# Optimization experiments

Measured on AMD Instinct MI355X. Metric: run time of the kernel, lower is better.

The kernel has to match this reference:

```python
import jax, jax.numpy as jnp
import numpy as np

T1 = -0.075410217
T2 = 0.0
T3 = 0.062207676


def my_squash2(s_j):
    # s_j: [B, 1, C, O, 1]; piecewise-linear rescale based on sorted channel-0 magnitudes.
    B, _, C, O, _ = s_j.shape
    f = s_j[:, 0, :, 0, 0]                      # [B, C] first element of each capsule
    order = jnp.argsort(f, axis=1)
    srt = jnp.take_along_axis(f, order, axis=1)  # ascending sort per sample
    i1 = jnp.sum(srt < T1, axis=1, keepdims=True)
    i2 = jnp.sum(srt < T2, axis=1, keepdims=True)
    i3 = jnp.sum(srt < T3, axis=1, keepdims=True)
    pos = jnp.arange(C)[None, :]
    seg1 = -0.074520095 * srt + 0.349297946
    seg2 = -0.534473989 * srt + 0.27196494
    seg3 = 0.637642944 * srt + 0.295330779
    seg4 = 0.169344703 * srt + 0.353784456
    # faithful to torch slices [0:i1-1], [i1:i2-1], [i2:i3-1], [i3:9] (segment-end indices untouched)
    m1 = (i1 > 0) & (pos < i1 - 1)
    m2 = (i2 > 0) & (i2 > i1) & (pos >= i1) & (pos < i2 - 1)
    m3 = (i3 > 0) & (i3 > i2) & (pos >= i2) & (pos < i3 - 1)
    m4 = (i3 < C) & (pos >= i3) & (pos < C - 1)
    new_srt = jnp.where(m1, seg1, jnp.where(m2, seg2, jnp.where(m3, seg3, jnp.where(m4, seg4, srt))))
    inv = jnp.argsort(order, axis=1)
    new_f = jnp.take_along_axis(new_srt, inv, axis=1)  # unsort back to capsule order
    # torch code mutates s_j in place: channel 0 of each capsule becomes new_f
    s_mut = s_j.at[:, 0, :, 0, 0].set(new_f)
    scale = new_f[:, None, :, None, None]            # expanded over out_channels
    return scale * s_mut, s_mut


def setup_inputs() -> dict:
    key = jax.random.key(0)
    k0, k1, k2, k3 = jax.random.split(key, 4)
    B, R, C, O, I = 100, 1152, 10, 16, 8
    return {
        "x0": jax.random.normal(k0, (B, R, I), dtype=jnp.float32),
        "x1": jax.random.normal(k1, (B, R, I), dtype=jnp.float32),
        "x2": jax.random.normal(k2, (B, 1, 28, 28), dtype=jnp.float32),
        "W": jax.random.normal(k3, (1, R, C, O, I), dtype=jnp.float32),
        "train_or_test": 0,
        "epch": 0,
    }


def reference(x0, x1, x2, W, train_or_test, epch):
    B, R, I = x0.shape
    C, O = W.shape[2], W.shape[3]
    squashed_u = jnp.broadcast_to(x0[:, :, None, :, None], (B, R, C, I, 1))
    # u_hat[b,r,c,o] = sum_i W[0,r,c,o,i] * x0[b,r,i]
    u_hat = jnp.einsum('rcoi,bri->brco', W[0], x0)[..., None]  # [B,R,C,O,1]
    b_ij = jnp.zeros((1, R, C, 1), dtype=x0.dtype)
    num_iterations = 3
    for it in range(num_iterations):
        c_ij = jax.nn.softmax(b_ij, axis=1)                    # over routes
        c_full = jnp.broadcast_to(c_ij, (B, R, C, 1))[..., None]
        s_j = jnp.sum(c_full * u_hat, axis=1, keepdims=True)   # [B,1,C,O,1]
        v_j, s_mut = my_squash2(s_j)
        if it < num_iterations - 1:
            a = jnp.einsum('brco,bco->brc', u_hat[..., 0], v_j[:, 0, :, :, 0])
            b_ij = b_ij + jnp.mean(a, axis=0)[None, :, :, None]
    Wb = jnp.broadcast_to(W, (B,) + W.shape[1:])
    return (v_j[:, 0], c_full, Wb, squashed_u, x1, x2, s_mut[:, 0])
```

## Files before the change

### kernel.cpp

```cpp
#include <hip/hip_runtime.h>

#define B 100
#define R 1152
#define C 10
#define O 16
#define I 8
#define RI 9216
#define RC2 2304
#define RCHUNK 16
#define NRC 72
#define KCH 128

#define T1c (-0.075410217f)
#define T3c (0.062207676f)

typedef float f4raw __attribute__((ext_vector_type(4)));
static __device__ __forceinline__ void nt_store4(const float4& v, float4* p) {
    __builtin_nontemporal_store(*(const f4raw*)&v, (f4raw*)p);
}

#define WS_BCOL 0
#define WS_CSM  11520
#define WS_PART 23040
#define WS_VOB  1175040

#define O_VJ 0
#define O_CF 4000
#define O_WB 292000
#define O_SQ 37156000
#define O_X1 39460000
#define O_X2 39690400
#define O_SM 39710000

#define U_WB 7200
#define U_SQ 563
#define U_X1 57
#define U_TOT 7825

__device__ void stream_unit(int u, const float4* __restrict__ W4,
                            const float4* __restrict__ x04,
                            const float4* __restrict__ x14,
                            const float4* __restrict__ x24,
                            float4* __restrict__ out) {
    const int t = threadIdx.x;
    if (u < U_WB) {
        int wchunk = u % 1440, bg = u / 1440;
        int idx = wchunk * 256 + t;
        float4 v = W4[idx];
        float4* dst = out + O_WB + (size_t)bg * 20 * 368640 + idx;
        #pragma unroll
        for (int b = 0; b < 20; b++) { nt_store4(v, dst); dst += 368640; }
    } else if (u < U_WB + U_SQ) {
        int s = u - U_WB;
        int m0 = s * 4096, m1 = m0 + 4096; if (m1 > 2304000) m1 = 2304000;
        for (int m = m0 + t; m < m1; m += 256) {
            float4 v = x04[(m / 20) * 2 + (m & 1)];
            nt_store4(v, &out[O_SQ + m]);
        }
    } else if (u < U_WB + U_SQ + U_X1) {
        int s = u - U_WB - U_SQ;
        int m0 = s * 4096, m1 = m0 + 4096; if (m1 > 230400) m1 = 230400;
        for (int m = m0 + t; m < m1; m += 256) nt_store4(x14[m], &out[O_X1 + m]);
    } else {
        int s = u - U_WB - U_SQ - U_X1;
        int m0 = s * 4096, m1 = m0 + 4096; if (m1 > 19600) m1 = 19600;
        for (int m = m0 + t; m < m1; m += 256) nt_store4(x24[m], &out[O_X2 + m]);
    }
}

__global__ __launch_bounds__(256) void k_gemm(const float* __restrict__ Wg,
                                              const float* __restrict__ x0,
                                              float* __restrict__ ws,
                                              const float4* __restrict__ x14,
                                              const float4* __restrict__ x24,
                                              float4* __restrict__ out,
                                              int it, int ubase) {
    const int t = threadIdx.x;
    const float4* x04 = (const float4*)x0;
    if (blockIdx.x >= 720) {
        stream_unit(ubase + (blockIdx.x - 720), (const float4*)Wg, x04, x14, x24, out);
        return;
    }
    const int rc = blockIdx.x % NRC, c = blockIdx.x / NRC;
    const int r0 = rc * RCHUNK;
    __shared__ float red[256];
    __shared__ float cw[RCHUNK];
    __shared__ __align__(16) float lw[KCH * O];
    __shared__ float2 tpp[16][104];

    if (it > 0) {
        const float* bcol = ws + WS_BCOL + c * R;
        float lm = -3.4e38f;
        for (int r = t; r < R; r += 256) lm = fmaxf(lm, bcol[r]);
        red[t] = lm; __syncthreads();
        for (int s = 128; s > 0; s >>= 1) { if (t < s) red[t] = fmaxf(red[t], red[t + s]); __syncthreads(); }
        const float m = red[0]; __syncthreads();
        float ls = 0.f;
        for (int r = t; r < R; r += 256) ls += expf(bcol[r] - m);
        red[t] = ls; __syncthreads();
        for (int s = 128; s > 0; s >>= 1) { if (t < s) red[t] += red[t + s]; __syncthreads(); }
        const float sinv = 1.f / red[0];
        if (t < RCHUNK) cw[t] = expf(bcol[r0 + t] - m) * sinv;
        if (it == 2 && rc == 0) {
            for (int r = t; r < R; r += 256)
                ws[WS_CSM + r * C + c] = expf(bcol[r] - m) * sinv;
        }
    } else {
        if (t < RCHUNK) cw[t] = 1.0f / 1152.0f;
    }
    __syncthreads();

    for (int j = t; j < KCH * O; j += 256) {
        int rr = j >> 7;
        int rem = j & 127;
        int o = rem >> 3, i = rem & 7;
        lw[((rr * I + i) << 4) + o] = cw[rr] * Wg[((size_t)(r0 + rr) * C + c) * 128 + rem];
    }

    const int bl = t & 63, og = t >> 6;
    int b2 = bl + 64; if (b2 > 103) b2 = 103;
    float4 a0 = {0, 0, 0, 0}, a1 = {0, 0, 0, 0};
    for (int p = 0; p < 4; p++) {
        __syncthreads();
        int colbase = r0 * 2 + p * 8;
        for (int e = t; e < 800; e += 256) {
            int b = e >> 3, q = e & 7;
            float4 v = x04[(size_t)b * RC2 + colbase + q];
            tpp[q * 2 + 0][b] = make_float2(v.x, v.y);
            tpp[q * 2 + 1][b] = make_float2(v.z, v.w);
        }
        if (p == 0 && t < 64) tpp[t >> 2][100 + (t & 3)] = make_float2(0.f, 0.f);
        __syncthreads();
        const float4* lwp = (const float4*)lw + p * 128;
        #pragma unroll 8
        for (int k2 = 0; k2 < 16; k2++) {
            float2 xv0 = tpp[k2][bl];
            float2 xv1 = tpp[k2][b2];
            float4 wa = lwp[k2 * 8 + og];
            float4 wb = lwp[k2 * 8 + 4 + og];
            a0.x += xv0.x * wa.x + xv0.y * wb.x;
            a0.y += xv0.x * wa.y + xv0.y * wb.y;
            a0.z += xv0.x * wa.z + xv0.y * wb.z;
            a0.w += xv0.x * wa.w + xv0.y * wb.w;
            a1.x += xv1.x * wa.x + xv1.y * wb.x;
            a1.y += xv1.x * wa.y + xv1.y * wb.y;
            a1.z += xv1.x * wa.z + xv1.y * wb.z;
            a1.w += xv1.x * wa.w + xv1.y * wb.w;
        }
    }
    float4* part4 = (float4*)(ws + WS_PART);
    int base = ((c * NRC + rc) * B + bl) * 4 + og;
    part4[base] = a0;
    if (bl < 36) part4[base + 256] = a1;
}

__global__ __launch_bounds__(256) void k_squash(float* __restrict__ ws) {
    const int t = threadIdx.x;
    const int b = blockIdx.x;
    __shared__ float sl[160];
    __shared__ float nf[C];
    if (t < 160) {
        int c = t >> 4, o = t & 15;
        float s = 0.f;
        const float* p = ws + WS_PART + ((size_t)c * NRC * B + b) * 16 + o;
        #pragma unroll 8
        for (int rc = 0; rc < NRC; rc++) s += p[rc * 1600];
        sl[t] = s;
    }
    __syncthreads();
    if (t < C) {
        float fv[C];
        #pragma unroll
        for (int c2 = 0; c2 < C; c2++) fv[c2] = sl[c2 * O];
        float mine = sl[t * O];
        int rank = 0, i1 = 0, i2 = 0, i3 = 0;
        #pragma unroll
        for (int c2 = 0; c2 < C; c2++) {
            rank += (fv[c2] < mine) || (fv[c2] == mine && c2 < t);
            i1 += fv[c2] < T1c;
            i2 += fv[c2] < 0.0f;
            i3 += fv[c2] < T3c;
        }
        float nv = mine;
        if (i1 > 0 && rank < i1 - 1)                               nv = -0.074520095f * mine + 0.349297946f;
        else if (i2 > 0 && i2 > i1 && rank >= i1 && rank < i2 - 1) nv = -0.534473989f * mine + 0.27196494f;
        else if (i3 > 0 && i3 > i2 && rank >= i2 && rank < i3 - 1) nv = 0.637642944f * mine + 0.295330779f;
        else if (i3 < C && rank >= i3 && rank < C - 1)             nv = 0.169344703f * mine + 0.353784456f;
        nf[t] = nv;
    }
    __syncthreads();
    if (t < 160) {
        int c = t >> 4, o = t & 15;
        float smut = (o == 0) ? nf[c] : sl[t];
        ws[WS_VOB + t * B + b] = nf[c] * smut;
    }
}

__global__ __launch_bounds__(256) void k_agree(const float* __restrict__ Wg,
                                               const float* __restrict__ x0,
                                               float* __restrict__ ws,
                                               const float4* __restrict__ x14,
                                               const float4* __restrict__ x24,
                                               float4* __restrict__ out,
                                               int it, int ubase) {
    const int t = threadIdx.x;
    if (blockIdx.x >= R) {
        stream_unit(ubase + (blockIdx.x - R), (const float4*)Wg, (const float4*)x0, x14, x24, out);
        return;
    }
    const int r = blockIdx.x;
    __shared__ __align__(16) float vt[3200];
    __shared__ __align__(16) float xs[800];
    __shared__ __align__(16) float arr[1280];
    const float4* x04 = (const float4*)x0;
    const float4* vob4 = (const float4*)(ws + WS_VOB);
    if (t < 200) {
        int b = t >> 1, half = t & 1;
        float4 v = x04[(size_t)b * RC2 + r * 2 + half];
        xs[(half * 4 + 0) * B + b] = v.x; xs[(half * 4 + 1) * B + b] = v.y;
        xs[(half * 4 + 2) * B + b] = v.z; xs[(half * 4 + 3) * B + b] = v.w;
    }
    const int i = t & 7, co0 = t >> 3;
    const float4* xs4 = (const float4*)(xs + i * B);
    const float4* vt4 = (const float4*)(vt + co0 * B);
    float4* vtw = (float4*)vt;
    for (int ch = 0; ch < 5; ch++) {
        __syncthreads();
        for (int j = t; j < 800; j += 256) vtw[j] = vob4[ch * 800 + j];
        __syncthreads();
        float q = 0.f;
        #pragma unroll
        for (int b4 = 0; b4 < 25; b4++) {
            float4 xv = xs4[b4];
            float4 vv = vt4[b4];
            q += xv.x * vv.x + xv.y * vv.y + xv.z * vv.z + xv.w * vv.w;
        }
        int co = ch * 32 + co0;
        arr[co * I + i] = q * Wg[(size_t)r * 1280 + co * I + i];
    }
    __syncthreads();
    if (t < C) {
        const float4* a4 = (const float4*)(arr + t * 128);
        float d = 0.f;
        #pragma unroll
        for (int m2 = 0; m2 < 32; m2++) { float4 v4 = a4[m2]; d += v4.x + v4.y + v4.z + v4.w; }
        float* dst = ws + WS_BCOL + t * R + r;
        float val = d * (1.0f / B);
        if (it == 0) *dst = val; else *dst += val;
    }
}

__global__ __launch_bounds__(256) void k_out(const float* __restrict__ x0,
                                             const float* __restrict__ x1,
                                             const float* __restrict__ x2,
                                             float* __restrict__ ws,
                                             const float* __restrict__ Wg,
                                             float4* __restrict__ out) {
    const int bid = blockIdx.x, t = threadIdx.x;
    if (bid < B) {
        const int b = bid;
        __shared__ float sl[160];
        __shared__ float nf[C];
        __shared__ __align__(16) float vv[160];
        __shared__ __align__(16) float sm[160];
        if (t < 160) {
            int c = t >> 4, o = t & 15;
            float s = 0.f;
            const float* p = ws + WS_PART + ((size_t)c * NRC * B + b) * 16 + o;
            #pragma unroll 8
            for (int rc = 0; rc < NRC; rc++) s += p[rc * 1600];
            sl[t] = s;
        }
        __syncthreads();
        if (t < C) {
            float fv[C];
            #pragma unroll
            for (int c2 = 0; c2 < C; c2++) fv[c2] = sl[c2 * O];
            float mine = sl[t * O];
            int rank = 0, i1 = 0, i2 = 0, i3 = 0;
            #pragma unroll
            for (int c2 = 0; c2 < C; c2++) {
                rank += (fv[c2] < mine) || (fv[c2] == mine && c2 < t);
                i1 += fv[c2] < T1c;
                i2 += fv[c2] < 0.0f;
                i3 += fv[c2] < T3c;
            }
            float nv = mine;
            if (i1 > 0 && rank < i1 - 1)                               nv = -0.074520095f * mine + 0.349297946f;
            else if (i2 > 0 && i2 > i1 && rank >= i1 && rank < i2 - 1) nv = -0.534473989f * mine + 0.27196494f;
            else if (i3 > 0 && i3 > i2 && rank >= i2 && rank < i3 - 1) nv = 0.637642944f * mine + 0.295330779f;
            else if (i3 < C && rank >= i3 && rank < C - 1)             nv = 0.169344703f * mine + 0.353784456f;
            nf[t] = nv;
        }
        __syncthreads();
        if (t < 160) {
            int c = t >> 4, o = t & 15;
            float smut = (o == 0) ? nf[c] : sl[t];
            sm[t] = smut;
            vv[t] = nf[c] * smut;
        }
        __syncthreads();
        if (t < 40) {
            nt_store4(((const float4*)vv)[t], &out[O_VJ + b * 40 + t]);
            nt_store4(((const float4*)sm)[t], &out[O_SM + b * 40 + t]);
        }
    }
    const float4* cs4 = (const float4*)(ws + WS_CSM);
    for (int j = bid * 256 + t; j < 288000; j += 2048 * 256)
        nt_store4(cs4[j % 2880], &out[O_CF + j]);
    for (int k = 0; k < 3; k++) {
        int u = 1800 + bid + k * 2048;
        if (u < U_TOT)
            stream_unit(u, (const float4*)Wg, (const float4*)x0,
                        (const float4*)x1, (const float4*)x2, out);
    }
}

extern "C" void kernel_launch(void* const* d_in, const int* in_sizes, int n_in,
                              void* d_out, int out_size, void* d_ws, size_t ws_size,
                              hipStream_t stream) {
    (void)in_sizes; (void)n_in; (void)out_size; (void)ws_size;
    const float* x0 = (const float*)d_in[0];
    const float* x1 = (const float*)d_in[1];
    const float* x2 = (const float*)d_in[2];
    const float* Wg = (const float*)d_in[3];
    const float4* x14 = (const float4*)x1;
    const float4* x24 = (const float4*)x2;
    float* ws = (float*)d_ws;
    float4* out = (float4*)d_out;

    hipLaunchKernelGGL(k_gemm,   dim3(720 + 400), dim3(256), 0, stream, Wg, x0, ws, x14, x24, out, 0, 0);
    hipLaunchKernelGGL(k_squash, dim3(100), dim3(256), 0, stream, ws);
    hipLaunchKernelGGL(k_agree,  dim3(1152 + 300), dim3(256), 0, stream, Wg, x0, ws, x14, x24, out, 0, 400);
    hipLaunchKernelGGL(k_gemm,   dim3(720 + 400), dim3(256), 0, stream, Wg, x0, ws, x14, x24, out, 1, 700);
    hipLaunchKernelGGL(k_squash, dim3(100), dim3(256), 0, stream, ws);
    hipLaunchKernelGGL(k_agree,  dim3(1152 + 300), dim3(256), 0, stream, Wg, x0, ws, x14, x24, out, 1, 1100);
    hipLaunchKernelGGL(k_gemm,   dim3(720 + 400), dim3(256), 0, stream, Wg, x0, ws, x14, x24, out, 2, 1400);
    hipLaunchKernelGGL(k_out,    dim3(2048), dim3(256), 0, stream, x0, x1, x2, ws, Wg, out);
}
```

Before: 221.7 us.

## Fuse squash into agreement kernel and enlarge route chunks to drop launches

```diff
diff --git a/kernel.cpp b/kernel.cpp
--- a/kernel.cpp
+++ b/kernel.cpp
@@ -7,9 +7,9 @@
 #define I 8
 #define RI 9216
 #define RC2 2304
-#define RCHUNK 16
-#define NRC 72
-#define KCH 128
+#define RCHUNK 48
+#define NRC 24
+#define KCH 384
 
 #define T1c (-0.075410217f)
 #define T3c (0.062207676f)
@@ -22,7 +22,7 @@
 #define WS_BCOL 0
 #define WS_CSM  11520
 #define WS_PART 23040
-#define WS_VOB  1175040
+#define WS_PARTF 407040
 
 #define O_VJ 0
 #define O_CF 4000
@@ -77,8 +77,8 @@
                                               int it, int ubase) {
     const int t = threadIdx.x;
     const float4* x04 = (const float4*)x0;
-    if (blockIdx.x >= 720) {
-        stream_unit(ubase + (blockIdx.x - 720), (const float4*)Wg, x04, x14, x24, out);
+    if (blockIdx.x >= 240) {
+        stream_unit(ubase + (blockIdx.x - 240), (const float4*)Wg, x04, x14, x24, out);
         return;
     }
     const int rc = blockIdx.x % NRC, c = blockIdx.x / NRC;
@@ -120,7 +120,7 @@
     const int bl = t & 63, og = t >> 6;
     int b2 = bl + 64; if (b2 > 103) b2 = 103;
     float4 a0 = {0, 0, 0, 0}, a1 = {0, 0, 0, 0};
-    for (int p = 0; p < 4; p++) {
+    for (int p = 0; p < 12; p++) {
         __syncthreads();
         int colbase = r0 * 2 + p * 8;
         for (int e = t; e < 800; e += 256) {
@@ -152,47 +152,9 @@
     int base = ((c * NRC + rc) * B + bl) * 4 + og;
     part4[base] = a0;
     if (bl < 36) part4[base + 256] = a1;
-}
-
-__global__ __launch_bounds__(256) void k_squash(float* __restrict__ ws) {
-    const int t = threadIdx.x;
-    const int b = blockIdx.x;
-    __shared__ float sl[160];
-    __shared__ float nf[C];
-    if (t < 160) {
-        int c = t >> 4, o = t & 15;
-        float s = 0.f;
-        const float* p = ws + WS_PART + ((size_t)c * NRC * B + b) * 16 + o;
-        #pragma unroll 8
-        for (int rc = 0; rc < NRC; rc++) s += p[rc * 1600];
-        sl[t] = s;
-    }
-    __syncthreads();
-    if (t < C) {
-        float fv[C];
-        #pragma unroll
-        for (int c2 = 0; c2 < C; c2++) fv[c2] = sl[c2 * O];
-        float mine = sl[t * O];
-        int rank = 0, i1 = 0, i2 = 0, i3 = 0;
-        #pragma unroll
-        for (int c2 = 0; c2 < C; c2++) {
-            rank += (fv[c2] < mine) || (fv[c2] == mine && c2 < t);
-            i1 += fv[c2] < T1c;
-            i2 += fv[c2] < 0.0f;
-            i3 += fv[c2] < T3c;
-        }
-        float nv = mine;
-        if (i1 > 0 && rank < i1 - 1)                               nv = -0.074520095f * mine + 0.349297946f;
-        else if (i2 > 0 && i2 > i1 && rank >= i1 && rank < i2 - 1) nv = -0.534473989f * mine + 0.27196494f;
-        else if (i3 > 0 && i3 > i2 && rank >= i2 && rank < i3 - 1) nv = 0.637642944f * mine + 0.295330779f;
-        else if (i3 < C && rank >= i3 && rank < C - 1)             nv = 0.169344703f * mine + 0.353784456f;
-        nf[t] = nv;
-    }
-    __syncthreads();
-    if (t < 160) {
-        int c = t >> 4, o = t & 15;
-        float smut = (o == 0) ? nf[c] : sl[t];
-        ws[WS_VOB + t * B + b] = nf[c] * smut;
+    if (og == 0) {
+        ws[WS_PARTF + (c * NRC + rc) * B + bl] = a0.x;
+        if (bl < 36) ws[WS_PARTF + (c * NRC + rc) * B + bl + 64] = a1.x;
     }
 }
 
@@ -204,29 +166,75 @@
                                                float4* __restrict__ out,
                                                int it, int ubase) {
     const int t = threadIdx.x;
-    if (blockIdx.x >= R) {
-        stream_unit(ubase + (blockIdx.x - R), (const float4*)Wg, (const float4*)x0, x14, x24, out);
+    if (blockIdx.x >= 180) {
+        stream_unit(ubase + (blockIdx.x - 180), (const float4*)Wg, (const float4*)x0, x14, x24, out);
         return;
     }
-    const int r = blockIdx.x;
+    const int rg = blockIdx.x / 5, ch = blockIdx.x % 5;
+    const int rbase = rg * 32;
+    __shared__ float fs[1000];
+    __shared__ float nf2[200];
     __shared__ __align__(16) float vt[3200];
     __shared__ __align__(16) float xs[800];
-    __shared__ __align__(16) float arr[1280];
+    __shared__ __align__(16) float arr[256];
     const float4* x04 = (const float4*)x0;
-    const float4* vob4 = (const float4*)(ws + WS_VOB);
+
+    for (int j = t; j < 1000; j += 256) {
+        int c = j / 100, b = j - c * 100;
+        const float* p = ws + WS_PARTF + c * (NRC * B) + b;
+        float s = 0.f;
+        #pragma unroll 8
+        for (int rc = 0; rc < NRC; rc++) s += p[rc * B];
+        fs[j] = s;
+    }
+    __syncthreads();
     if (t < 200) {
-        int b = t >> 1, half = t & 1;
-        float4 v = x04[(size_t)b * RC2 + r * 2 + half];
-        xs[(half * 4 + 0) * B + b] = v.x; xs[(half * 4 + 1) * B + b] = v.y;
-        xs[(half * 4 + 2) * B + b] = v.z; xs[(half * 4 + 3) * B + b] = v.w;
-    }
-    const int i = t & 7, co0 = t >> 3;
+        int cl = t / 100, b = t - cl * 100;
+        int c = ch * 2 + cl;
+        float mine = fs[c * 100 + b];
+        int rank = 0, i1 = 0, i2 = 0, i3 = 0;
+        #pragma unroll
+        for (int c2 = 0; c2 < C; c2++) {
+            float f2 = fs[c2 * 100 + b];
+            rank += (f2 < mine) || (f2 == mine && c2 < c);
+            i1 += f2 < T1c;
+            i2 += f2 < 0.0f;
+            i3 += f2 < T3c;
+        }
+        float nv = mine;
+        if (i1 > 0 && rank < i1 - 1)                               nv = -0.074520095f * mine + 0.349297946f;
+        else if (i2 > 0 && i2 > i1 && rank >= i1 && rank < i2 - 1) nv = -0.534473989f * mine + 0.27196494f;
+        else if (i3 > 0 && i3 > i2 && rank >= i2 && rank < i3 - 1) nv = 0.637642944f * mine + 0.295330779f;
+        else if (i3 < C && rank >= i3 && rank < C - 1)             nv = 0.169344703f * mine + 0.353784456f;
+        nf2[t] = nv;
+    }
+    __syncthreads();
+    for (int j = t; j < 3200; j += 256) {
+        int cl = j / 1600, rem = j - cl * 1600;
+        int b = rem >> 4, o = rem & 15;
+        int c = ch * 2 + cl;
+        const float* p = ws + WS_PART + (size_t)(c * NRC) * 1600 + b * 16 + o;
+        float s = 0.f;
+        #pragma unroll 8
+        for (int rc = 0; rc < NRC; rc++) s += p[rc * 1600];
+        float nfv = nf2[cl * 100 + b];
+        float smut = (o == 0) ? nfv : s;
+        vt[(cl * 16 + o) * 100 + b] = nfv * smut;
+    }
+
+    const int i = t & 7, co = t >> 3;
     const float4* xs4 = (const float4*)(xs + i * B);
-    const float4* vt4 = (const float4*)(vt + co0 * B);
-    float4* vtw = (float4*)vt;
-    for (int ch = 0; ch < 5; ch++) {
-        __syncthreads();
-        for (int j = t; j < 800; j += 256) vtw[j] = vob4[ch * 800 + j];
+    const float4* vt4 = (const float4*)(vt + co * B);
+    const int cg = ch * 2 + (co >> 4), og = co & 15;
+    for (int rr = 0; rr < 32; rr++) {
+        const int r = rbase + rr;
+        __syncthreads();
+        if (t < 200) {
+            int b = t >> 1, half = t & 1;
+            float4 v = x04[(size_t)b * RC2 + r * 2 + half];
+            xs[(half * 4 + 0) * B + b] = v.x; xs[(half * 4 + 1) * B + b] = v.y;
+            xs[(half * 4 + 2) * B + b] = v.z; xs[(half * 4 + 3) * B + b] = v.w;
+        }
         __syncthreads();
         float q = 0.f;
         #pragma unroll
@@ -235,18 +243,17 @@
             float4 vv = vt4[b4];
             q += xv.x * vv.x + xv.y * vv.y + xv.z * vv.z + xv.w * vv.w;
         }
-        int co = ch * 32 + co0;
-        arr[co * I + i] = q * Wg[(size_t)r * 1280 + co * I + i];
-    }
-    __syncthreads();
-    if (t < C) {
-        const float4* a4 = (const float4*)(arr + t * 128);
-        float d = 0.f;
-        #pragma unroll
-        for (int m2 = 0; m2 < 32; m2++) { float4 v4 = a4[m2]; d += v4.x + v4.y + v4.z + v4.w; }
-        float* dst = ws + WS_BCOL + t * R + r;
-        float val = d * (1.0f / B);
-        if (it == 0) *dst = val; else *dst += val;
+        arr[co * I + i] = q * Wg[(size_t)r * 1280 + (cg * 16 + og) * 8 + i];
+        __syncthreads();
+        if (t < 2) {
+            const float4* a4 = (const float4*)(arr + t * 128);
+            float d = 0.f;
+            #pragma unroll
+            for (int m2 = 0; m2 < 32; m2++) { float4 v4 = a4[m2]; d += v4.x + v4.y + v4.z + v4.w; }
+            float* dst = ws + WS_BCOL + (ch * 2 + t) * R + r;
+            float val = d * (1.0f / B);
+            if (it == 0) *dst = val; else *dst += val;
+        }
     }
 }
 
@@ -308,8 +315,8 @@
     const float4* cs4 = (const float4*)(ws + WS_CSM);
     for (int j = bid * 256 + t; j < 288000; j += 2048 * 256)
         nt_store4(cs4[j % 2880], &out[O_CF + j]);
-    for (int k = 0; k < 3; k++) {
-        int u = 1800 + bid + k * 2048;
+    for (int k = 0; k < 2; k++) {
+        int u = 4080 + bid + k * 2048;
         if (u < U_TOT)
             stream_unit(u, (const float4*)Wg, (const float4*)x0,
                         (const float4*)x1, (const float4*)x2, out);
@@ -329,12 +336,10 @@
     float* ws = (float*)d_ws;
     float4* out = (float4*)d_out;
 
-    hipLaunchKernelGGL(k_gemm,   dim3(720 + 400), dim3(256), 0, stream, Wg, x0, ws, x14, x24, out, 0, 0);
-    hipLaunchKernelGGL(k_squash, dim3(100), dim3(256), 0, stream, ws);
-    hipLaunchKernelGGL(k_agree,  dim3(1152 + 300), dim3(256), 0, stream, Wg, x0, ws, x14, x24, out, 0, 400);
-    hipLaunchKernelGGL(k_gemm,   dim3(720 + 400), dim3(256), 0, stream, Wg, x0, ws, x14, x24, out, 1, 700);
-    hipLaunchKernelGGL(k_squash, dim3(100), dim3(256), 0, stream, ws);
-    hipLaunchKernelGGL(k_agree,  dim3(1152 + 300), dim3(256), 0, stream, Wg, x0, ws, x14, x24, out, 1, 1100);
-    hipLaunchKernelGGL(k_gemm,   dim3(720 + 400), dim3(256), 0, stream, Wg, x0, ws, x14, x24, out, 2, 1400);
-    hipLaunchKernelGGL(k_out,    dim3(2048), dim3(256), 0, stream, x0, x1, x2, ws, Wg, out);
-}
+    hipLaunchKernelGGL(k_gemm,  dim3(240 + 760), dim3(256), 0, stream, Wg, x0, ws, x14, x24, out, 0, 0);
+    hipLaunchKernelGGL(k_agree, dim3(180 + 900), dim3(256), 0, stream, Wg, x0, ws, x14, x24, out, 0, 760);
+    hipLaunchKernelGGL(k_gemm,  dim3(240 + 760), dim3(256), 0, stream, Wg, x0, ws, x14, x24, out, 1, 1660);
+    hipLaunchKernelGGL(k_agree, dim3(180 + 900), dim3(256), 0, stream, Wg, x0, ws, x14, x24, out, 1, 2420);
+    hipLaunchKernelGGL(k_gemm,  dim3(240 + 760), dim3(256), 0, stream, Wg, x0, ws, x14, x24, out, 2, 3320);
+    hipLaunchKernelGGL(k_out,   dim3(2048), dim3(256), 0, stream, x0, x1, x2, ws, Wg, out);
+}
```

Result: slower. 369.9 us (+66.8%).

## Fuse all routing phases into one persistent kernel with grid barriers

Applied to the files above, without the earlier changes.

```diff
diff --git a/kernel.cpp b/kernel.cpp
--- a/kernel.cpp
+++ b/kernel.cpp
@@ -11,6 +11,9 @@
 #define NRC 72
 #define KCH 128
 
+#define NB 720
+#define GRID 1024
+
 #define T1c (-0.075410217f)
 #define T3c (0.062207676f)
 
@@ -19,10 +22,11 @@
     __builtin_nontemporal_store(*(const f4raw*)&v, (f4raw*)p);
 }
 
-#define WS_BCOL 0
-#define WS_CSM  11520
-#define WS_PART 23040
-#define WS_VOB  1175040
+#define WS_CNT  0
+#define WS_BCOL 64
+#define WS_CSM  11584
+#define WS_PART 23104
+#define WS_VOB  1175104
 
 #define O_VJ 0
 #define O_CF 4000
@@ -36,6 +40,7 @@
 #define U_SQ 563
 #define U_X1 57
 #define U_TOT 7825
+#define STREAM_BASE 3873
 
 __device__ void stream_unit(int u, const float4* __restrict__ W4,
                             const float4* __restrict__ x04,
@@ -68,25 +73,28 @@
     }
 }
 
-__global__ __launch_bounds__(256) void k_gemm(const float* __restrict__ Wg,
-                                              const float* __restrict__ x0,
-                                              float* __restrict__ ws,
-                                              const float4* __restrict__ x14,
-                                              const float4* __restrict__ x24,
-                                              float4* __restrict__ out,
-                                              int it, int ubase) {
-    const int t = threadIdx.x;
-    const float4* x04 = (const float4*)x0;
-    if (blockIdx.x >= 720) {
-        stream_unit(ubase + (blockIdx.x - 720), (const float4*)Wg, x04, x14, x24, out);
-        return;
-    }
-    const int rc = blockIdx.x % NRC, c = blockIdx.x / NRC;
+static __device__ __forceinline__ void rbar(unsigned* cnt, unsigned target) {
+    __syncthreads();
+    if (threadIdx.x == 0) {
+        __hip_atomic_fetch_add(cnt, 1u, __ATOMIC_RELEASE, __HIP_MEMORY_SCOPE_AGENT);
+        while (__hip_atomic_load(cnt, __ATOMIC_RELAXED, __HIP_MEMORY_SCOPE_AGENT) < target)
+            __builtin_amdgcn_s_sleep(16);
+        __builtin_amdgcn_fence(__ATOMIC_ACQUIRE, "agent");
+    }
+    __syncthreads();
+}
+
+#define TPP(k2, b) tpp[(k2) * 104 + (b)]
+
+static __device__ void phase_g(int bk, int t, const float* __restrict__ Wg,
+                               const float4* __restrict__ x04,
+                               float* __restrict__ ws, int it, float* smem) {
+    const int rc = bk % NRC, c = bk / NRC;
     const int r0 = rc * RCHUNK;
-    __shared__ float red[256];
-    __shared__ float cw[RCHUNK];
-    __shared__ __align__(16) float lw[KCH * O];
-    __shared__ float2 tpp[16][104];
+    float* red = smem;
+    float* cw  = smem + 256;
+    float* lw  = smem + 272;
+    float2* tpp = (float2*)(smem + 2320);
 
     if (it > 0) {
         const float* bcol = ws + WS_BCOL + c * R;
@@ -126,16 +134,16 @@
         for (int e = t; e < 800; e += 256) {
             int b = e >> 3, q = e & 7;
             float4 v = x04[(size_t)b * RC2 + colbase + q];
-            tpp[q * 2 + 0][b] = make_float2(v.x, v.y);
-            tpp[q * 2 + 1][b] = make_float2(v.z, v.w);
-        }
-        if (p == 0 && t < 64) tpp[t >> 2][100 + (t & 3)] = make_float2(0.f, 0.f);
+            TPP(q * 2 + 0, b) = make_float2(v.x, v.y);
+            TPP(q * 2 + 1, b) = make_float2(v.z, v.w);
+        }
+        if (p == 0 && t < 64) TPP(t >> 2, 100 + (t & 3)) = make_float2(0.f, 0.f);
         __syncthreads();
         const float4* lwp = (const float4*)lw + p * 128;
         #pragma unroll 8
         for (int k2 = 0; k2 < 16; k2++) {
-            float2 xv0 = tpp[k2][bl];
-            float2 xv1 = tpp[k2][b2];
+            float2 xv0 = TPP(k2, bl);
+            float2 xv1 = TPP(k2, b2);
             float4 wa = lwp[k2 * 8 + og];
             float4 wb = lwp[k2 * 8 + 4 + og];
             a0.x += xv0.x * wa.x + xv0.y * wb.x;
@@ -152,13 +160,12 @@
     int base = ((c * NRC + rc) * B + bl) * 4 + og;
     part4[base] = a0;
     if (bl < 36) part4[base + 256] = a1;
-}
-
-__global__ __launch_bounds__(256) void k_squash(float* __restrict__ ws) {
-    const int t = threadIdx.x;
-    const int b = blockIdx.x;
-    __shared__ float sl[160];
-    __shared__ float nf[C];
+    __syncthreads();
+}
+
+static __device__ void phase_s(int b, int t, float* __restrict__ ws, float* smem) {
+    float* sl = smem;
+    float* nf = smem + 160;
     if (t < 160) {
         int c = t >> 4, o = t & 15;
         float s = 0.f;
@@ -194,26 +201,17 @@
         float smut = (o == 0) ? nf[c] : sl[t];
         ws[WS_VOB + t * B + b] = nf[c] * smut;
     }
-}
-
-__global__ __launch_bounds__(256) void k_agree(const float* __restrict__ Wg,
-                                               const float* __restrict__ x0,
-                                               float* __restrict__ ws,
-                                               const float4* __restrict__ x14,
-                                               const float4* __restrict__ x24,
-                                               float4* __restrict__ out,
-                                               int it, int ubase) {
-    const int t = threadIdx.x;
-    if (blockIdx.x >= R) {
-        stream_unit(ubase + (blockIdx.x - R), (const float4*)Wg, (const float4*)x0, x14, x24, out);
-        return;
-    }
-    const int r = blockIdx.x;
-    __shared__ __align__(16) float vt[3200];
-    __shared__ __align__(16) float xs[800];
-    __shared__ __align__(16) float arr[1280];
-    const float4* x04 = (const float4*)x0;
+    __syncthreads();
+}
+
+static __device__ void phase_a_one(int r, int t, const float* __restrict__ Wg,
+                                   const float4* __restrict__ x04,
+                                   float* __restrict__ ws, int it, float* smem) {
+    float* vt  = smem;
+    float* xs  = smem + 3200;
+    float* arr = smem + 4000;
     const float4* vob4 = (const float4*)(ws + WS_VOB);
+    __syncthreads();
     if (t < 200) {
         int b = t >> 1, half = t & 1;
         float4 v = x04[(size_t)b * RC2 + r * 2 + half];
@@ -250,19 +248,51 @@
     }
 }
 
-__global__ __launch_bounds__(256) void k_out(const float* __restrict__ x0,
-                                             const float* __restrict__ x1,
-                                             const float* __restrict__ x2,
-                                             float* __restrict__ ws,
-                                             const float* __restrict__ Wg,
-                                             float4* __restrict__ out) {
-    const int bid = blockIdx.x, t = threadIdx.x;
-    if (bid < B) {
-        const int b = bid;
-        __shared__ float sl[160];
-        __shared__ float nf[C];
-        __shared__ __align__(16) float vv[160];
-        __shared__ __align__(16) float sm[160];
+__global__ __launch_bounds__(256, 4) void k_all(const float* __restrict__ x0,
+                                                const float* __restrict__ x1,
+                                                const float* __restrict__ x2,
+                                                const float* __restrict__ Wg,
+                                                float* __restrict__ ws,
+                                                float4* __restrict__ out) {
+    const int bk = blockIdx.x, t = threadIdx.x;
+    __shared__ __align__(16) float smem[5664];
+    unsigned* cnt = (unsigned*)ws;
+    const float4* W4  = (const float4*)Wg;
+    const float4* x04 = (const float4*)x0;
+    const float4* x14 = (const float4*)x1;
+    const float4* x24 = (const float4*)x2;
+
+    if (bk >= NB) {
+        int s = bk - NB;
+        #pragma unroll 1
+        for (int n = 0; n < 13; n++)
+            stream_unit(STREAM_BASE + s * 13 + n, W4, x04, x14, x24, out);
+        return;
+    }
+
+    phase_g(bk, t, Wg, x04, ws, 0, smem);
+    rbar(cnt, NB * 1);
+    if (bk < B) phase_s(bk, t, ws, smem);
+    rbar(cnt, NB * 2);
+    phase_a_one(bk, t, Wg, x04, ws, 0, smem);
+    if (bk < 432) phase_a_one(720 + bk, t, Wg, x04, ws, 0, smem);
+    rbar(cnt, NB * 3);
+    phase_g(bk, t, Wg, x04, ws, 1, smem);
+    rbar(cnt, NB * 4);
+    if (bk < B) phase_s(bk, t, ws, smem);
+    rbar(cnt, NB * 5);
+    phase_a_one(bk, t, Wg, x04, ws, 1, smem);
+    if (bk < 432) phase_a_one(720 + bk, t, Wg, x04, ws, 1, smem);
+    rbar(cnt, NB * 6);
+    phase_g(bk, t, Wg, x04, ws, 2, smem);
+    rbar(cnt, NB * 7);
+
+    if (bk < B) {
+        const int b = bk;
+        float* sl = smem;
+        float* nf = smem + 160;
+        float* vv = smem + 176;
+        float* sm = smem + 336;
         if (t < 160) {
             int c = t >> 4, o = t & 15;
             float s = 0.f;
@@ -306,13 +336,12 @@
         }
     }
     const float4* cs4 = (const float4*)(ws + WS_CSM);
-    for (int j = bid * 256 + t; j < 288000; j += 2048 * 256)
+    for (int j = bk * 256 + t; j < 288000; j += NB * 256)
         nt_store4(cs4[j % 2880], &out[O_CF + j]);
-    for (int k = 0; k < 3; k++) {
-        int u = 1800 + bid + k * 2048;
-        if (u < U_TOT)
-            stream_unit(u, (const float4*)Wg, (const float4*)x0,
-                        (const float4*)x1, (const float4*)x2, out);
+    #pragma unroll 1
+    for (int n = 0; n < 7; n++) {
+        int u = bk * 7 + n;
+        if (u < STREAM_BASE) stream_unit(u, W4, x04, x14, x24, out);
     }
 }
 
@@ -324,17 +353,9 @@
     const float* x1 = (const float*)d_in[1];
     const float* x2 = (const float*)d_in[2];
     const float* Wg = (const float*)d_in[3];
-    const float4* x14 = (const float4*)x1;
-    const float4* x24 = (const float4*)x2;
     float* ws = (float*)d_ws;
     float4* out = (float4*)d_out;
 
-    hipLaunchKernelGGL(k_gemm,   dim3(720 + 400), dim3(256), 0, stream, Wg, x0, ws, x14, x24, out, 0, 0);
-    hipLaunchKernelGGL(k_squash, dim3(100), dim3(256), 0, stream, ws);
-    hipLaunchKernelGGL(k_agree,  dim3(1152 + 300), dim3(256), 0, stream, Wg, x0, ws, x14, x24, out, 0, 400);
-    hipLaunchKernelGGL(k_gemm,   dim3(720 + 400), dim3(256), 0, stream, Wg, x0, ws, x14, x24, out, 1, 700);
-    hipLaunchKernelGGL(k_squash, dim3(100), dim3(256), 0, stream, ws);
-    hipLaunchKernelGGL(k_agree,  dim3(1152 + 300), dim3(256), 0, stream, Wg, x0, ws, x14, x24, out, 1, 1100);
-    hipLaunchKernelGGL(k_gemm,   dim3(720 + 400), dim3(256), 0, stream, Wg, x0, ws, x14, x24, out, 2, 1400);
-    hipLaunchKernelGGL(k_out,    dim3(2048), dim3(256), 0, stream, x0, x1, x2, ws, Wg, out);
-}
+    hipMemsetAsync(d_ws, 0, 256, stream);
+    hipLaunchKernelGGL(k_all, dim3(GRID), dim3(256), 0, stream, x0, x1, x2, Wg, ws, out);
+}
```

Result: slower. 637.4 us (+187.5%).
